# Optimization experiments

Measured on AMD Instinct MI355X. Metric: run time of the kernel, lower is better.

Reference implementation:

```python
import jax, jax.numpy as jnp
import numpy as np

HIDDEN = 1024
HEADS = 16
HEAD_DIM = HIDDEN // HEADS


def setup_inputs() -> dict:
    key = jax.random.key(0)
    ks = jax.random.split(key, 5)
    x = jax.random.normal(ks[0], (4, 2048, HIDDEN), dtype=jnp.float32)
    s = 1.0 / np.sqrt(HIDDEN)
    W_qkv = jax.random.normal(ks[1], (HIDDEN, 3 * HIDDEN), dtype=jnp.float32) * s
    b_qkv = jax.random.normal(ks[2], (3 * HIDDEN,), dtype=jnp.float32) * s
    W_out = jax.random.normal(ks[3], (HIDDEN, HIDDEN), dtype=jnp.float32) * s
    b_out = jax.random.normal(ks[4], (HIDDEN,), dtype=jnp.float32) * s
    return {"x": x, "W_qkv": W_qkv, "b_qkv": b_qkv, "W_out": W_out, "b_out": b_out}


def reference(x, W_qkv, b_qkv, W_out, b_out):
    B, S, _ = x.shape
    qkv = x @ W_qkv + b_qkv                       # [B,S,3H]
    qkv = qkv.reshape(B, S, 3, HEADS, HEAD_DIM)
    q, k, v = jnp.moveaxis(qkv, 2, 0)             # each [B,S,nh,hd]
    scale = 1.0 / np.sqrt(HEAD_DIM)
    scores = jnp.einsum('bqhd,bkhd->bhqk', q, k) * scale
    probs = jax.nn.softmax(scores, axis=-1)       # dropout p=0 (eval): identity
    attn = jnp.einsum('bhqk,bkhd->bqhd', probs, v)
    attn = attn.reshape(B, S, HIDDEN)
    return attn @ W_out + b_out
```

## Files before the change

### kernel.cpp

```cpp
#include <hip/hip_runtime.h>

#define SEQ    2048
#define BATCH  4
#define HID    1024
#define NH     16
#define MTOT   (BATCH * SEQ)

typedef __attribute__((ext_vector_type(8)))  short          short8;
typedef __attribute__((ext_vector_type(4)))  float          f32x4;
typedef __attribute__((ext_vector_type(16))) float          f32x16;
typedef __attribute__((ext_vector_type(8)))  unsigned short ushort8v;

#define QSCL 0.125f

__device__ __forceinline__ float bf2f(unsigned short u) {
    return __uint_as_float(((unsigned int)u) << 16);
}
__device__ __forceinline__ unsigned short f2bf(float f) {
    unsigned int u = __float_as_uint(f);
    u += 0x7fffu + ((u >> 16) & 1u);
    return (unsigned short)(u >> 16);
}
__device__ __forceinline__ unsigned int pk2bf(float lo, float hi) {
    unsigned int ul = __float_as_uint(lo) + 0x8000u;
    unsigned int uh = __float_as_uint(hi) + 0x8000u;
    return __builtin_amdgcn_perm(uh, ul, 0x07060302u);
}

__device__ __forceinline__ void gl_lds16(const void* g, void* l) {
    __builtin_amdgcn_global_load_lds(
        (__attribute__((address_space(1))) void*)g,
        (__attribute__((address_space(3))) void*)l, 16, 0, 0);
}

__device__ __forceinline__ int swz64(int row, int col) {
    return row * 64 + ((((col >> 3) ^ (row & 7))) << 3) + (col & 7);
}

__device__ __forceinline__ int gidx64(int row, int kq) {
    return (row * 8 + ((kq + (row & 7)) & 7)) * 8;
}

__global__ __launch_bounds__(256)
void cvt_x(const float* __restrict__ x, unsigned short* __restrict__ xb)
{
    const size_t i = ((size_t)blockIdx.x * 256 + threadIdx.x) * 4;
    const float4 f = *(const float4*)(x + i);
    uint2 u;
    u.x = pk2bf(f.x, f.y);
    u.y = pk2bf(f.z, f.w);
    *(uint2*)(xb + i) = u;
}

__global__ __launch_bounds__(256)
void transpose_cvt(const float* __restrict__ W, unsigned short* __restrict__ Wt,
                   int K, int N)
{
    __shared__ unsigned short T[32][33];
    const int n0 = blockIdx.x * 32, k0 = blockIdx.y * 32;
    const int tr = threadIdx.x >> 3, tc = (threadIdx.x & 7) * 4;
    const float4 f = *(const float4*)(W + (size_t)(k0 + tr) * N + n0 + tc);
    T[tr][tc + 0] = f2bf(f.x);
    T[tr][tc + 1] = f2bf(f.y);
    T[tr][tc + 2] = f2bf(f.z);
    T[tr][tc + 3] = f2bf(f.w);
    __syncthreads();
    ushort4 u;
    u.x = T[tc + 0][tr]; u.y = T[tc + 1][tr];
    u.z = T[tc + 2][tr]; u.w = T[tc + 3][tr];
    *(ushort4*)(Wt + (size_t)(n0 + tr) * K + k0 + tc) = u;
}

template<bool OUTF32, bool VSPLIT>
__global__ __launch_bounds__(256)
void gemm_mfma(const unsigned short* __restrict__ A,
               const unsigned short* __restrict__ Bt,
               const float* __restrict__ bias, void* __restrict__ Cptr,
               unsigned short* __restrict__ Vt,
               int lda, int ldc, int K)
{
    __shared__ unsigned short As[128 * 64];
    __shared__ unsigned short Bs[128 * 64];

    const int tid = threadIdx.x;
    const int wave = tid >> 6, lane = tid & 63;
    const int quad = lane >> 4, lm = lane & 15;
    const int wm = wave & 1, wn = wave >> 1;
    const int m0 = blockIdx.y * 128, n0 = blockIdx.x * 128;

    const unsigned short* aSrc[4];
    const unsigned short* bSrc[4];
    unsigned short* aDst[4];
    unsigned short* bDst[4];
    #pragma unroll
    for (int j = 0; j < 4; ++j) {
        const int g = (wave * 4 + j) * 64 + lane;
        const int row = g >> 3;
        const int kq = ((g & 7) - (row & 7)) & 7;
        aSrc[j] = A  + (size_t)(m0 + row) * lda + kq * 8;
        bSrc[j] = Bt + (size_t)(n0 + row) * K   + kq * 8;
        aDst[j] = &As[g * 8];
        bDst[j] = &Bs[g * 8];
    }

    f32x4 acc[4][4];
    #pragma unroll
    for (int i = 0; i < 4; ++i)
        #pragma unroll
        for (int j = 0; j < 4; ++j)
            acc[i][j] = (f32x4){0.f, 0.f, 0.f, 0.f};

    int aOff[2][4], bOff[2][4];
    #pragma unroll
    for (int h = 0; h < 2; ++h)
        #pragma unroll
        for (int i = 0; i < 4; ++i) {
            aOff[h][i] = gidx64(wm * 64 + i * 16 + lm, h * 4 + quad);
            bOff[h][i] = gidx64(wn * 64 + i * 16 + lm, h * 4 + quad);
        }

    for (int k0 = 0; k0 < K; k0 += 64) {
        __syncthreads();
        #pragma unroll
        for (int j = 0; j < 4; ++j) gl_lds16(aSrc[j] + k0, aDst[j]);
        #pragma unroll
        for (int j = 0; j < 4; ++j) gl_lds16(bSrc[j] + k0, bDst[j]);
        __syncthreads();

        #pragma unroll
        for (int h = 0; h < 2; ++h) {
            short8 af[4], bf[4];
            #pragma unroll
            for (int i = 0; i < 4; ++i) af[i] = *(const short8*)&As[aOff[h][i]];
            #pragma unroll
            for (int j = 0; j < 4; ++j) bf[j] = *(const short8*)&Bs[bOff[h][j]];
            #pragma unroll
            for (int i = 0; i < 4; ++i)
                #pragma unroll
                for (int j = 0; j < 4; ++j)
                    acc[i][j] = __builtin_amdgcn_mfma_f32_16x16x32_bf16(
                        af[i], bf[j], acc[i][j], 0, 0, 0);
        }
    }

    float bj[4];
    #pragma unroll
    for (int j = 0; j < 4; ++j) bj[j] = bias[n0 + wn * 64 + j * 16 + lm];

    #pragma unroll
    for (int i = 0; i < 4; ++i) {
        #pragma unroll
        for (int j = 0; j < 4; ++j) {
            const int col = n0 + wn * 64 + j * 16 + lm;
            #pragma unroll
            for (int rr = 0; rr < 4; ++rr) {
                const int row = m0 + wm * 64 + i * 16 + quad * 4 + rr;
                float v = acc[i][j][rr] + bj[j];
                if (VSPLIT) {
                    if (col >= 2048) {
                        const int dg = col - 2048;
                        const int b = row >> 11, s = row & 2047;
                        Vt[((size_t)b * 1024 + dg) * 2048 + s] = f2bf(v);
                    } else {
                        if (col < 1024) v *= QSCL;
                        ((unsigned short*)Cptr)[(size_t)row * ldc + col] = f2bf(v);
                    }
                } else if (OUTF32) {
                    ((float*)Cptr)[(size_t)row * ldc + col] = v;
                } else {
                    ((unsigned short*)Cptr)[(size_t)row * ldc + col] = f2bf(v);
                }
            }
        }
    }
}

__global__ __launch_bounds__(256, 2)
void attn_mfma(unsigned short* __restrict__ qk,
               const unsigned short* __restrict__ Vt)
{
    const int qt = blockIdx.x, hh = blockIdx.y, b = blockIdx.z;
    const size_t row0 = (size_t)b * SEQ;
    const int tid = threadIdx.x;
    const int wave = tid >> 6, lane = tid & 63;
    const int l5 = lane >> 5, lm = lane & 31;

    __shared__ unsigned short Ks[64 * 64];
    __shared__ unsigned short Vst[64 * 64];
    __shared__ unsigned short Ps[4][64 * 64];

    const int qbase = qt * 256 + wave * 64;

    short8 qf[2][4];
    #pragma unroll
    for (int qg = 0; qg < 2; ++qg)
        #pragma unroll
        for (int ks = 0; ks < 4; ++ks)
            qf[qg][ks] = *(const short8*)(
                qk + (row0 + qbase + qg * 32 + lm) * 2048 + hh * 64 + ks * 16 + l5 * 8);

    f32x16 oacc[2][2];
    #pragma unroll
    for (int dg = 0; dg < 2; ++dg)
        #pragma unroll
        for (int qg = 0; qg < 2; ++qg)
            #pragma unroll
            for (int e = 0; e < 16; ++e) oacc[dg][qg][e] = 0.f;
    float lrun[2] = {0.f, 0.f};

    const int srow = tid >> 2;
    const int scol = (tid & 3) * 16;

    const unsigned short* kbase = qk + 1024 + hh * 64;
    const unsigned short* vbase = Vt + ((size_t)b * 1024 + hh * 64 + srow) * 2048;

    ushort8v kp0, kp1, vp0, vp1;
    {
        const unsigned short* kp = kbase + (row0 + srow) * 2048 + scol;
        kp0 = *(const ushort8v*)kp;  kp1 = *(const ushort8v*)(kp + 8);
        vp0 = *(const ushort8v*)(vbase + scol);
        vp1 = *(const ushort8v*)(vbase + scol + 8);
    }

    for (int kt = 0; kt < SEQ; kt += 64) {
        __syncthreads();
        *(ushort8v*)&Ks[swz64(srow, scol)]      = kp0;
        *(ushort8v*)&Ks[swz64(srow, scol + 8)]  = kp1;
        *(ushort8v*)&Vst[swz64(srow, scol)]     = vp0;
        *(ushort8v*)&Vst[swz64(srow, scol + 8)] = vp1;
        __syncthreads();

        {
            const int nk = (kt + 64 < SEQ) ? kt + 64 : kt;
            const unsigned short* kp = kbase + (row0 + nk + srow) * 2048 + scol;
            kp0 = *(const ushort8v*)kp;  kp1 = *(const ushort8v*)(kp + 8);
            vp0 = *(const ushort8v*)(vbase + nk + scol);
            vp1 = *(const ushort8v*)(vbase + nk + scol + 8);
        }

        #pragma unroll
        for (int kg = 0; kg < 2; ++kg) {
            f32x16 s[2];
            #pragma unroll
            for (int qg = 0; qg < 2; ++qg)
                #pragma unroll
                for (int e = 0; e < 16; ++e) s[qg][e] = 0.f;
            #pragma unroll
            for (int ks = 0; ks < 4; ++ks) {
                const short8 aK =
                    *(const short8*)&Ks[swz64(kg * 32 + lm, ks * 16 + l5 * 8)];
                #pragma unroll
                for (int qg = 0; qg < 2; ++qg)
                    s[qg] = __builtin_amdgcn_mfma_f32_32x32x16_bf16(
                        aK, qf[qg][ks], s[qg], 0, 0, 0);
            }
            #pragma unroll
            for (int qg = 0; qg < 2; ++qg) {
                float ls = 0.f;
                #pragma unroll
                for (int rg = 0; rg < 4; ++rg) {
                    const float p0 = __expf(s[qg][rg * 4 + 0]);
                    const float p1 = __expf(s[qg][rg * 4 + 1]);
                    const float p2 = __expf(s[qg][rg * 4 + 2]);
                    const float p3 = __expf(s[qg][rg * 4 + 3]);
                    ls += (p0 + p1) + (p2 + p3);
                    uint2 pk;
                    pk.x = pk2bf(p0, p1);
                    pk.y = pk2bf(p2, p3);
                    *(uint2*)&Ps[wave][swz64(qg * 32 + lm,
                                             kg * 32 + rg * 8 + l5 * 4)] = pk;
                }
                lrun[qg] += ls;
            }
        }

        #pragma unroll
        for (int ks = 0; ks < 4; ++ks) {
            const short8 aV0 = *(const short8*)&Vst[swz64(lm,      ks * 16 + l5 * 8)];
            const short8 aV1 = *(const short8*)&Vst[swz64(32 + lm, ks * 16 + l5 * 8)];
            #pragma unroll
            for (int qg = 0; qg < 2; ++qg) {
                const short8 bP =
                    *(const short8*)&Ps[wave][swz64(qg * 32 + lm, ks * 16 + l5 * 8)];
                oacc[0][qg] = __builtin_amdgcn_mfma_f32_32x32x16_bf16(
                    aV0, bP, oacc[0][qg], 0, 0, 0);
                oacc[1][qg] = __builtin_amdgcn_mfma_f32_32x32x16_bf16(
                    aV1, bP, oacc[1][qg], 0, 0, 0);
            }
        }
    }

    float linv[2];
    #pragma unroll
    for (int qg = 0; qg < 2; ++qg) {
        const float lt = lrun[qg] + __shfl_xor(lrun[qg], 32);
        linv[qg] = 1.f / lt;
    }

    #pragma unroll
    for (int dg = 0; dg < 2; ++dg)
        #pragma unroll
        for (int qg = 0; qg < 2; ++qg) {
            unsigned short* orow =
                qk + (row0 + qbase + qg * 32 + lm) * 2048 + hh * 64;
            #pragma unroll
            for (int rg = 0; rg < 4; ++rg) {
                const int d0 = dg * 32 + rg * 8 + l5 * 4;
                ushort4 st;
                st.x = f2bf(oacc[dg][qg][rg * 4 + 0] * linv[qg]);
                st.y = f2bf(oacc[dg][qg][rg * 4 + 1] * linv[qg]);
                st.z = f2bf(oacc[dg][qg][rg * 4 + 2] * linv[qg]);
                st.w = f2bf(oacc[dg][qg][rg * 4 + 3] * linv[qg]);
                *(ushort4*)(orow + d0) = st;
            }
        }
}

__global__ __launch_bounds__(256)
void qproj(const float* __restrict__ A, const float* __restrict__ W,
           const float* __restrict__ bias, unsigned short* __restrict__ outus)
{
    __shared__ float As[64][17];
    __shared__ float Bs[16][64];
    const int tid = threadIdx.x;
    const int tx = tid & 15, ty = tid >> 4;
    const int m0 = blockIdx.y * 64, n0 = blockIdx.x * 64;
    const int ar = tid >> 2, ac = (tid & 3) * 4;
    const int br = tid >> 4, bc = (tid & 15) * 4;
    float acc[4][4] = {{0.f}};
    for (int k0 = 0; k0 < HID; k0 += 16) {
        const float4 av = *(const float4*)(A + (size_t)(m0 + ar) * HID + k0 + ac);
        As[ar][ac + 0] = av.x; As[ar][ac + 1] = av.y;
        As[ar][ac + 2] = av.z; As[ar][ac + 3] = av.w;
        *(float4*)&Bs[br][bc] =
            *(const float4*)(W + (size_t)(k0 + br) * 3072 + n0 + bc);
        __syncthreads();
        #pragma unroll
        for (int kk = 0; kk < 16; ++kk) {
            float a[4];
            #pragma unroll
            for (int i = 0; i < 4; ++i) a[i] = As[ty * 4 + i][kk];
            const float4 b4 = *(const float4*)&Bs[kk][tx * 4];
            const float bv[4] = {b4.x, b4.y, b4.z, b4.w};
            #pragma unroll
            for (int i = 0; i < 4; ++i)
                #pragma unroll
                for (int j = 0; j < 4; ++j)
                    acc[i][j] = fmaf(a[i], bv[j], acc[i][j]);
        }
        __syncthreads();
    }
    float bb[4];
    #pragma unroll
    for (int j = 0; j < 4; ++j) bb[j] = bias[n0 + tx * 4 + j];
    #pragma unroll
    for (int i = 0; i < 4; ++i) {
        ushort4 st;
        st.x = f2bf(acc[i][0] + bb[0]); st.y = f2bf(acc[i][1] + bb[1]);
        st.z = f2bf(acc[i][2] + bb[2]); st.w = f2bf(acc[i][3] + bb[3]);
        *(ushort4*)(outus + (size_t)(m0 + ty * 4 + i) * 2048 + 1024 + n0 + tx * 4) = st;
    }
}

__global__ __launch_bounds__(256)
void kv_inplace(const float* __restrict__ W, const float* __restrict__ bias,
                unsigned short* __restrict__ xu)
{
    const float* xf = (const float*)xu;
    __shared__ unsigned short Asb[16][1032];
    __shared__ float Bs[16][68];
    const int tid = threadIdx.x;
    const int m0 = blockIdx.x * 16;
    const int tx = tid & 15, ty = tid >> 4;
    #pragma unroll 4
    for (int i = 0; i < 16; ++i) {
        const float4 v = *(const float4*)(xf + (size_t)(m0 + i) * HID + tid * 4);
        ushort4 s;
        s.x = f2bf(v.x); s.y = f2bf(v.y); s.z = f2bf(v.z); s.w = f2bf(v.w);
        *(ushort4*)&Asb[i][tid * 4] = s;
    }
    __syncthreads();
    for (int n0 = 0; n0 < 2048; n0 += 64) {
        float acc[4] = {0.f, 0.f, 0.f, 0.f};
        for (int k0 = 0; k0 < HID; k0 += 16) {
            *(float4*)&Bs[ty][tx * 4] =
                *(const float4*)(W + (size_t)(k0 + ty) * 3072 + 1024 + n0 + tx * 4);
            __syncthreads();
            #pragma unroll
            for (int kk = 0; kk < 16; ++kk) {
                const float a = bf2f(Asb[ty][k0 + kk]);
                const float4 b4 = *(const float4*)&Bs[kk][tx * 4];
                acc[0] = fmaf(a, b4.x, acc[0]); acc[1] = fmaf(a, b4.y, acc[1]);
                acc[2] = fmaf(a, b4.z, acc[2]); acc[3] = fmaf(a, b4.w, acc[3]);
            }
            __syncthreads();
        }
        const int n = n0 + tx * 4;
        ushort4 s;
        s.x = f2bf(acc[0] + bias[1024 + n + 0]);
        s.y = f2bf(acc[1] + bias[1024 + n + 1]);
        s.z = f2bf(acc[2] + bias[1024 + n + 2]);
        s.w = f2bf(acc[3] + bias[1024 + n + 3]);
        *(ushort4*)(xu + (size_t)(m0 + ty) * 2048 + n) = s;
    }
}

__global__ __launch_bounds__(256)
void attn_fwd(const unsigned short* __restrict__ xu,
              unsigned short* __restrict__ outus)
{
    const int qt = blockIdx.x, h = blockIdx.y, b = blockIdx.z;
    const int s0 = qt * 16;
    const size_t row0 = (size_t)b * SEQ;
    const int tid = threadIdx.x;
    const int qi = tid >> 4, tj = tid & 15;
    __shared__ float Ksh[64][68];
    __shared__ float Vsh[64][68];
    __shared__ float Psh[16][68];
    float qreg[64];
    {
        const uint4* qp =
            (const uint4*)(outus + (row0 + s0 + qi) * 2048 + 1024 + h * 64);
        #pragma unroll
        for (int i = 0; i < 8; ++i) {
            uint4 u = qp[i];
            const unsigned int w[4] = {u.x, u.y, u.z, u.w};
            #pragma unroll
            for (int j = 0; j < 4; ++j) {
                qreg[i * 8 + j * 2 + 0] = __uint_as_float(w[j] << 16) * 0.125f;
                qreg[i * 8 + j * 2 + 1] = __uint_as_float(w[j] & 0xffff0000u) * 0.125f;
            }
        }
    }
    float mrun = -1e30f, lrunv = 0.f;
    float oacc[4] = {0.f, 0.f, 0.f, 0.f};
    const int lr = tid >> 3, lc = (tid & 7) * 8;
    for (int kt = 0; kt < SEQ; kt += 64) {
        __syncthreads();
        #pragma unroll
        for (int half = 0; half < 2; ++half) {
            const int r = lr + half * 32;
            const size_t rowoff = (row0 + kt + r) * 2048 + h * 64 + lc;
            uint4 ku = *(const uint4*)(xu + rowoff);
            uint4 vu = *(const uint4*)(xu + rowoff + 1024);
            float4 f0, f1;
            f0.x = __uint_as_float(ku.x << 16); f0.y = __uint_as_float(ku.x & 0xffff0000u);
            f0.z = __uint_as_float(ku.y << 16); f0.w = __uint_as_float(ku.y & 0xffff0000u);
            f1.x = __uint_as_float(ku.z << 16); f1.y = __uint_as_float(ku.z & 0xffff0000u);
            f1.z = __uint_as_float(ku.w << 16); f1.w = __uint_as_float(ku.w & 0xffff0000u);
            *(float4*)&Ksh[r][lc]     = f0;
            *(float4*)&Ksh[r][lc + 4] = f1;
            f0.x = __uint_as_float(vu.x << 16); f0.y = __uint_as_float(vu.x & 0xffff0000u);
            f0.z = __uint_as_float(vu.y << 16); f0.w = __uint_as_float(vu.y & 0xffff0000u);
            f1.x = __uint_as_float(vu.z << 16); f1.y = __uint_as_float(vu.z & 0xffff0000u);
            f1.z = __uint_as_float(vu.w << 16); f1.w = __uint_as_float(vu.w & 0xffff0000u);
            *(float4*)&Vsh[r][lc]     = f0;
            *(float4*)&Vsh[r][lc + 4] = f1;
        }
        __syncthreads();
        float sc[4];
        #pragma unroll
        for (int u = 0; u < 4; ++u) {
            const int kk = tj + 16 * u;
            float s = 0.f;
            #pragma unroll
            for (int d = 0; d < 64; ++d) s = fmaf(qreg[d], Ksh[kk][d], s);
            sc[u] = s;
        }
        float tmax = fmaxf(fmaxf(sc[0], sc[1]), fmaxf(sc[2], sc[3]));
        #pragma unroll
        for (int off = 8; off >= 1; off >>= 1)
            tmax = fmaxf(tmax, __shfl_xor(tmax, off, 16));
        const float mnew = fmaxf(mrun, tmax);
        const float alpha = __expf(mrun - mnew);
        float psum = 0.f;
        #pragma unroll
        for (int u = 0; u < 4; ++u) {
            const float p = __expf(sc[u] - mnew);
            Psh[qi][tj + 16 * u] = p;
            psum += p;
        }
        #pragma unroll
        for (int off = 8; off >= 1; off >>= 1)
            psum += __shfl_xor(psum, off, 16);
        lrunv = lrunv * alpha + psum;
        mrun = mnew;
        oacc[0] *= alpha; oacc[1] *= alpha; oacc[2] *= alpha; oacc[3] *= alpha;
        __syncthreads();
        #pragma unroll 8
        for (int kk = 0; kk < 64; ++kk) {
            const float p = Psh[qi][kk];
            const float4 v4 = *(const float4*)&Vsh[kk][tj * 4];
            oacc[0] = fmaf(p, v4.x, oacc[0]); oacc[1] = fmaf(p, v4.y, oacc[1]);
            oacc[2] = fmaf(p, v4.z, oacc[2]); oacc[3] = fmaf(p, v4.w, oacc[3]);
        }
    }
    const float inv = 1.f / lrunv;
    ushort4 st;
    st.x = f2bf(oacc[0] * inv); st.y = f2bf(oacc[1] * inv);
    st.z = f2bf(oacc[2] * inv); st.w = f2bf(oacc[3] * inv);
    *(ushort4*)(outus + (row0 + s0 + qi) * 2048 + h * 64 + tj * 4) = st;
}

__global__ __launch_bounds__(256)
void out_final(const float* __restrict__ W, const float* __restrict__ bias,
               unsigned short* __restrict__ outus)
{
    float* outf = (float*)outus;
    __shared__ unsigned short Asb[16][1032];
    __shared__ float Bs[16][68];
    const int tid = threadIdx.x;
    const int m0 = blockIdx.x * 16;
    const int tx = tid & 15, ty = tid >> 4;
    #pragma unroll 4
    for (int i = 0; i < 16; ++i)
        *(ushort4*)&Asb[i][tid * 4] =
            *(const ushort4*)(outus + (size_t)(m0 + i) * 2048 + tid * 4);
    __syncthreads();
    for (int n0 = 0; n0 < 1024; n0 += 64) {
        float acc[4] = {0.f, 0.f, 0.f, 0.f};
        for (int k0 = 0; k0 < HID; k0 += 16) {
            *(float4*)&Bs[ty][tx * 4] =
                *(const float4*)(W + (size_t)(k0 + ty) * HID + n0 + tx * 4);
            __syncthreads();
            #pragma unroll
            for (int kk = 0; kk < 16; ++kk) {
                const float a = bf2f(Asb[ty][k0 + kk]);
                const float4 b4 = *(const float4*)&Bs[kk][tx * 4];
                acc[0] = fmaf(a, b4.x, acc[0]); acc[1] = fmaf(a, b4.y, acc[1]);
                acc[2] = fmaf(a, b4.z, acc[2]); acc[3] = fmaf(a, b4.w, acc[3]);
            }
            __syncthreads();
        }
        const int n = n0 + tx * 4;
        float4 st;
        st.x = acc[0] + bias[n + 0]; st.y = acc[1] + bias[n + 1];
        st.z = acc[2] + bias[n + 2]; st.w = acc[3] + bias[n + 3];
        *(float4*)(outf + (size_t)(m0 + ty) * HID + n) = st;
    }
}

extern "C" void kernel_launch(void* const* d_in, const int* in_sizes, int n_in,
                              void* d_out, int out_size, void* d_ws, size_t ws_size,
                              hipStream_t stream) {
    const float* x     = (const float*)d_in[0];
    const float* W_qkv = (const float*)d_in[1];
    const float* b_qkv = (const float*)d_in[2];
    const float* W_out = (const float*)d_in[3];
    const float* b_out = (const float*)d_in[4];

    dim3 blk(256);

    if (ws_size >= (size_t)56 * 1024 * 1024) {
        unsigned short* qkbuf  = (unsigned short*)d_ws;
        unsigned short* vtbuf  = qkbuf + (size_t)MTOT * 2048;
        unsigned short* wqkv_t = vtbuf + (size_t)BATCH * NH * 64 * 2048;
        unsigned short* wout_t = wqkv_t + (size_t)3072 * 1024;
        unsigned short* xb     = (unsigned short*)d_out;

        cvt_x<<<dim3(MTOT * HID / 1024), blk, 0, stream>>>(x, xb);
        transpose_cvt<<<dim3(3072 / 32, 1024 / 32), blk, 0, stream>>>(
            W_qkv, wqkv_t, 1024, 3072);
        transpose_cvt<<<dim3(1024 / 32, 1024 / 32), blk, 0, stream>>>(
            W_out, wout_t, 1024, 1024);
        gemm_mfma<false, true><<<dim3(3072 / 128, MTOT / 128), blk, 0, stream>>>(
            xb, wqkv_t, b_qkv, (void*)qkbuf, vtbuf, 1024, 2048, 1024);
        attn_mfma<<<dim3(SEQ / 256, NH, BATCH), blk, 0, stream>>>(qkbuf, vtbuf);
        gemm_mfma<true, false><<<dim3(1024 / 128, MTOT / 128), blk, 0, stream>>>(
            qkbuf, wout_t, b_out, d_out, nullptr, 2048, 1024, 1024);
    } else {
        unsigned short* outus = (unsigned short*)d_out;
        unsigned short* xu    = (unsigned short*)d_in[0];
        qproj<<<dim3(HID / 64, MTOT / 64), blk, 0, stream>>>(x, W_qkv, b_qkv, outus);
        kv_inplace<<<dim3(MTOT / 16), blk, 0, stream>>>(W_qkv, b_qkv, xu);
        attn_fwd<<<dim3(SEQ / 16, NH, BATCH), blk, 0, stream>>>(xu, outus);
        out_final<<<dim3(MTOT / 16), blk, 0, stream>>>(W_out, b_out, outus);
    }
}
```

Before: 309.0 us.

## Keep softmax probabilities in registers and compute V^T with a dedicated transposed GEMM

The attention kernel no longer writes P to LDS and reads it back. It packs the exponentiated scores to bf16 in registers and rearranges them across half-waves with permlane32_swap to form the MFMA B operand directly. This removes the Ps shared buffer and its LDS traffic, which lowers LDS use and may allow higher occupancy. The QKV projection is also split: Q and K use the original GEMM, while V^T is produced by a separate GEMM that swaps the operands and applies a per-row bias, replacing the scattered strided transpose stores in the epilogue with coalesced ones.

```diff
diff --git a/kernel.cpp b/kernel.cpp
--- a/kernel.cpp
+++ b/kernel.cpp
@@ -10,6 +10,7 @@
 typedef __attribute__((ext_vector_type(4)))  float          f32x4;
 typedef __attribute__((ext_vector_type(16))) float          f32x16;
 typedef __attribute__((ext_vector_type(8)))  unsigned short ushort8v;
+typedef __attribute__((ext_vector_type(4)))  unsigned int   uint4v;
 
 #define QSCL 0.125f
 
@@ -71,12 +72,11 @@
     *(ushort4*)(Wt + (size_t)(n0 + tr) * K + k0 + tc) = u;
 }
 
-template<bool OUTF32, bool VSPLIT>
+template<bool OUTF32, bool VSPLIT, bool BIASROW>
 __global__ __launch_bounds__(256)
 void gemm_mfma(const unsigned short* __restrict__ A,
                const unsigned short* __restrict__ Bt,
                const float* __restrict__ bias, void* __restrict__ Cptr,
-               unsigned short* __restrict__ Vt,
                int lda, int ldc, int K)
 {
     __shared__ unsigned short As[128 * 64];
@@ -144,8 +144,18 @@
     }
 
     float bj[4];
-    #pragma unroll
-    for (int j = 0; j < 4; ++j) bj[j] = bias[n0 + wn * 64 + j * 16 + lm];
+    float br[4][4];
+    if constexpr (BIASROW) {
+        #pragma unroll
+        for (int i = 0; i < 4; ++i) {
+            const float4 t =
+                *(const float4*)(bias + m0 + wm * 64 + i * 16 + quad * 4);
+            br[i][0] = t.x; br[i][1] = t.y; br[i][2] = t.z; br[i][3] = t.w;
+        }
+    } else {
+        #pragma unroll
+        for (int j = 0; j < 4; ++j) bj[j] = bias[n0 + wn * 64 + j * 16 + lm];
+    }
 
     #pragma unroll
     for (int i = 0; i < 4; ++i) {
@@ -155,17 +165,11 @@
             #pragma unroll
             for (int rr = 0; rr < 4; ++rr) {
                 const int row = m0 + wm * 64 + i * 16 + quad * 4 + rr;
-                float v = acc[i][j][rr] + bj[j];
-                if (VSPLIT) {
-                    if (col >= 2048) {
-                        const int dg = col - 2048;
-                        const int b = row >> 11, s = row & 2047;
-                        Vt[((size_t)b * 1024 + dg) * 2048 + s] = f2bf(v);
-                    } else {
-                        if (col < 1024) v *= QSCL;
-                        ((unsigned short*)Cptr)[(size_t)row * ldc + col] = f2bf(v);
-                    }
-                } else if (OUTF32) {
+                float v = acc[i][j][rr] + (BIASROW ? br[i][rr] : bj[j]);
+                if constexpr (VSPLIT) {
+                    if (col < 1024) v *= QSCL;
+                    ((unsigned short*)Cptr)[(size_t)row * ldc + col] = f2bf(v);
+                } else if constexpr (OUTF32) {
                     ((float*)Cptr)[(size_t)row * ldc + col] = v;
                 } else {
                     ((unsigned short*)Cptr)[(size_t)row * ldc + col] = f2bf(v);
@@ -187,7 +191,6 @@
 
     __shared__ unsigned short Ks[64 * 64];
     __shared__ unsigned short Vst[64 * 64];
-    __shared__ unsigned short Ps[4][64 * 64];
 
     const int qbase = qt * 256 + wave * 64;
 
@@ -212,7 +215,8 @@
     const int scol = (tid & 3) * 16;
 
     const unsigned short* kbase = qk + 1024 + hh * 64;
-    const unsigned short* vbase = Vt + ((size_t)b * 1024 + hh * 64 + srow) * 2048;
+    const unsigned short* vbase =
+        Vt + (size_t)(hh * 64 + srow) * (size_t)MTOT + (size_t)b * SEQ;
 
     ushort8v kp0, kp1, vp0, vp1;
     {
@@ -240,22 +244,20 @@
 
         #pragma unroll
         for (int kg = 0; kg < 2; ++kg) {
+            short8 aK[4];
+            #pragma unroll
+            for (int ks = 0; ks < 4; ++ks)
+                aK[ks] = *(const short8*)&Ks[swz64(kg * 32 + lm, ks * 16 + l5 * 8)];
+
             f32x16 s[2];
             #pragma unroll
-            for (int qg = 0; qg < 2; ++qg)
+            for (int qg = 0; qg < 2; ++qg) {
                 #pragma unroll
                 for (int e = 0; e < 16; ++e) s[qg][e] = 0.f;
-            #pragma unroll
-            for (int ks = 0; ks < 4; ++ks) {
-                const short8 aK =
-                    *(const short8*)&Ks[swz64(kg * 32 + lm, ks * 16 + l5 * 8)];
                 #pragma unroll
-                for (int qg = 0; qg < 2; ++qg)
+                for (int ks = 0; ks < 4; ++ks)
                     s[qg] = __builtin_amdgcn_mfma_f32_32x32x16_bf16(
-                        aK, qf[qg][ks], s[qg], 0, 0, 0);
-            }
-            #pragma unroll
-            for (int qg = 0; qg < 2; ++qg) {
+                        aK[ks], qf[qg][ks], s[qg], 0, 0, 0);
                 float ls = 0.f;
                 #pragma unroll
                 for (int rg = 0; rg < 4; ++rg) {
@@ -263,29 +265,39 @@
                     const float p1 = __expf(s[qg][rg * 4 + 1]);
                     const float p2 = __expf(s[qg][rg * 4 + 2]);
                     const float p3 = __expf(s[qg][rg * 4 + 3]);
+                    s[qg][rg * 4 + 0] = p0; s[qg][rg * 4 + 1] = p1;
+                    s[qg][rg * 4 + 2] = p2; s[qg][rg * 4 + 3] = p3;
                     ls += (p0 + p1) + (p2 + p3);
-                    uint2 pk;
-                    pk.x = pk2bf(p0, p1);
-                    pk.y = pk2bf(p2, p3);
-                    *(uint2*)&Ps[wave][swz64(qg * 32 + lm,
-                                             kg * 32 + rg * 8 + l5 * 4)] = pk;
                 }
                 lrun[qg] += ls;
             }
-        }
-
-        #pragma unroll
-        for (int ks = 0; ks < 4; ++ks) {
-            const short8 aV0 = *(const short8*)&Vst[swz64(lm,      ks * 16 + l5 * 8)];
-            const short8 aV1 = *(const short8*)&Vst[swz64(32 + lm, ks * 16 + l5 * 8)];
-            #pragma unroll
-            for (int qg = 0; qg < 2; ++qg) {
-                const short8 bP =
-                    *(const short8*)&Ps[wave][swz64(qg * 32 + lm, ks * 16 + l5 * 8)];
-                oacc[0][qg] = __builtin_amdgcn_mfma_f32_32x32x16_bf16(
-                    aV0, bP, oacc[0][qg], 0, 0, 0);
-                oacc[1][qg] = __builtin_amdgcn_mfma_f32_32x32x16_bf16(
-                    aV1, bP, oacc[1][qg], 0, 0, 0);
+
+            #pragma unroll
+            for (int step = 0; step < 2; ++step) {
+                const int ks = kg * 2 + step;
+                const short8 aV0 =
+                    *(const short8*)&Vst[swz64(lm,      ks * 16 + l5 * 8)];
+                const short8 aV1 =
+                    *(const short8*)&Vst[swz64(32 + lm, ks * 16 + l5 * 8)];
+                #pragma unroll
+                for (int qg = 0; qg < 2; ++qg) {
+                    const int b0 = step * 8;
+                    const unsigned int u  = pk2bf(s[qg][b0 + 0], s[qg][b0 + 1]);
+                    const unsigned int vv = pk2bf(s[qg][b0 + 2], s[qg][b0 + 3]);
+                    const unsigned int u2 = pk2bf(s[qg][b0 + 4], s[qg][b0 + 5]);
+                    const unsigned int v2 = pk2bf(s[qg][b0 + 6], s[qg][b0 + 7]);
+                    const auto rA =
+                        __builtin_amdgcn_permlane32_swap(u,  u2, false, false);
+                    const auto rB =
+                        __builtin_amdgcn_permlane32_swap(vv, v2, false, false);
+                    uint4v wv;
+                    wv.x = rA[0]; wv.y = rB[0]; wv.z = rA[1]; wv.w = rB[1];
+                    const short8 bP = __builtin_bit_cast(short8, wv);
+                    oacc[0][qg] = __builtin_amdgcn_mfma_f32_32x32x16_bf16(
+                        aV0, bP, oacc[0][qg], 0, 0, 0);
+                    oacc[1][qg] = __builtin_amdgcn_mfma_f32_32x32x16_bf16(
+                        aV1, bP, oacc[1][qg], 0, 0, 0);
+                }
             }
         }
     }
@@ -554,7 +566,7 @@
     if (ws_size >= (size_t)56 * 1024 * 1024) {
         unsigned short* qkbuf  = (unsigned short*)d_ws;
         unsigned short* vtbuf  = qkbuf + (size_t)MTOT * 2048;
-        unsigned short* wqkv_t = vtbuf + (size_t)BATCH * NH * 64 * 2048;
+        unsigned short* wqkv_t = vtbuf + (size_t)1024 * MTOT;
         unsigned short* wout_t = wqkv_t + (size_t)3072 * 1024;
         unsigned short* xb     = (unsigned short*)d_out;
 
@@ -563,11 +575,14 @@
             W_qkv, wqkv_t, 1024, 3072);
         transpose_cvt<<<dim3(1024 / 32, 1024 / 32), blk, 0, stream>>>(
             W_out, wout_t, 1024, 1024);
-        gemm_mfma<false, true><<<dim3(3072 / 128, MTOT / 128), blk, 0, stream>>>(
-            xb, wqkv_t, b_qkv, (void*)qkbuf, vtbuf, 1024, 2048, 1024);
+        gemm_mfma<false, true, false><<<dim3(2048 / 128, MTOT / 128), blk, 0, stream>>>(
+            xb, wqkv_t, b_qkv, (void*)qkbuf, 1024, 2048, 1024);
+        gemm_mfma<false, false, true><<<dim3(MTOT / 128, 1024 / 128), blk, 0, stream>>>(
+            wqkv_t + (size_t)2048 * 1024, xb, b_qkv + 2048, (void*)vtbuf,
+            1024, MTOT, 1024);
         attn_mfma<<<dim3(SEQ / 256, NH, BATCH), blk, 0, stream>>>(qkbuf, vtbuf);
-        gemm_mfma<true, false><<<dim3(1024 / 128, MTOT / 128), blk, 0, stream>>>(
-            qkbuf, wout_t, b_out, d_out, nullptr, 2048, 1024, 1024);
+        gemm_mfma<true, false, false><<<dim3(1024 / 128, MTOT / 128), blk, 0, stream>>>(
+            qkbuf, wout_t, b_out, d_out, 2048, 1024, 1024);
     } else {
         unsigned short* outus = (unsigned short*)d_out;
         unsigned short* xu    = (unsigned short*)d_in[0];
```

Result: faster. 290.3 us (-6.1%).
